# Optimization experiments

Hardware: AMD Instinct MI355X
Metric: run time of the kernel (lower is better)

## Reference

```python
import jax, jax.numpy as jnp
import numpy as np

H = 16        # num_attention_heads
KV = 4        # num_key_value_heads
HD = 128      # head_dim = hidden // H
N_REP = H // KV
ROPE_THETA = 10000.0


def _rope_cos_sin(T, dtype):
    inv_freq = 1.0 / (ROPE_THETA ** (jnp.arange(0, HD, 2, dtype=jnp.float32) / HD))
    pos = jnp.arange(T, dtype=jnp.float32)
    freqs = pos[:, None] * inv_freq[None, :]            # [T, HD/2]
    emb = jnp.concatenate([freqs, freqs], axis=-1)      # [T, HD]
    return jnp.cos(emb).astype(dtype), jnp.sin(emb).astype(dtype)


def _rotate_half(t):
    t1, t2 = jnp.split(t, 2, axis=-1)
    return jnp.concatenate([-t2, t1], axis=-1)


def setup_inputs() -> dict:
    key = jax.random.key(0)
    k1, k2, k3 = jax.random.split(key, 3)
    B, T, C = 2, 2048, 2048
    x = jax.random.normal(k1, (B, T, C), dtype=jnp.float32)
    attention_mask = jnp.ones((B, T), dtype=jnp.float32)
    w_qkv = jax.random.normal(k2, ((H + 2 * KV) * HD, C), dtype=jnp.float32) * 0.02
    w_proj = jax.random.normal(k3, (C, C), dtype=jnp.float32) * 0.02
    return {"x": x, "attention_mask": attention_mask, "w_qkv": w_qkv, "w_proj": w_proj}


def reference(x, attention_mask, w_qkv, w_proj):
    B, T, C = x.shape
    dtype = x.dtype
    neg = jnp.finfo(dtype).min

    # additive mask: causal (-big above diagonal) + padding ((1-mask)*min)
    i = jnp.arange(T)
    causal = jnp.where(i[None, :] <= i[:, None], 0.0, neg).astype(dtype)  # [T,T]
    add_mask = (1.0 - attention_mask)[:, None, None, :] * neg + causal[None, None]  # [B,1,T,T]

    # fused QKV projection
    qkv = jnp.einsum('btc,oc->bto', x, w_qkv)
    q = qkv[..., : H * HD].reshape(B, T, H, HD)
    k = qkv[..., H * HD : (H + KV) * HD].reshape(B, T, KV, HD)
    v = qkv[..., (H + KV) * HD :].reshape(B, T, KV, HD)

    # RoPE on q and k
    cos, sin = _rope_cos_sin(T, dtype)
    cos = cos[None, :, None, :]
    sin = sin[None, :, None, :]
    q = q * cos + _rotate_half(q) * sin
    k = k * cos + _rotate_half(k) * sin

    # GQA: repeat_interleave KV heads
    k = jnp.repeat(k, N_REP, axis=2)  # [B,T,H,HD]
    v = jnp.repeat(v, N_REP, axis=2)

    # [B,H,T,HD]
    q, k, v = (jnp.transpose(t, (0, 2, 1, 3)) for t in (q, k, v))

    scores = jnp.einsum('bhqd,bhkd->bhqk', q, k) * (1.0 / np.sqrt(HD))
    att = jax.nn.softmax(scores + add_mask, axis=-1)
    y = jnp.einsum('bhqk,bhkd->bhqd', att, v)
    y = jnp.transpose(y, (0, 2, 1, 3)).reshape(B, T, C)
    return jnp.einsum('btc,oc->bto', y, w_proj)
```

## Files before the change

kernel.cpp:

```cpp
#include <hip/hip_runtime.h>
#include <hip/hip_bf16.h>
#include <stdint.h>

typedef unsigned short u16;
typedef __attribute__((ext_vector_type(4))) float f32x4;
typedef __attribute__((ext_vector_type(16))) float f32x16;
typedef __attribute__((ext_vector_type(8))) __bf16 bf16x8;

#define NB 2
#define NT 2048
#define NC 2048
#define NH 16
#define NKV 4
#define HD 128
#define NQKV 3072
#define SCALE2 0.12751739f

__device__ __forceinline__ u16 f2bf(float f) {
  union { float f; uint32_t u; } c; c.f = f;
  uint32_t u = c.u + 0x7fffu + ((c.u >> 16) & 1u);
  return (u16)(u >> 16);
}
__device__ __forceinline__ float bf2f(u16 h) {
  union { uint32_t u; float f; } c; c.u = ((uint32_t)h) << 16;
  return c.f;
}
__device__ __forceinline__ uint32_t packbf2(float a, float b) {
  return (uint32_t)f2bf(a) | ((uint32_t)f2bf(b) << 16);
}

__device__ __forceinline__ void gload16(const void* g, void* lds) {
  __builtin_amdgcn_global_load_lds(
      (__attribute__((address_space(1))) void*)(uintptr_t)g,
      (__attribute__((address_space(3))) void*)(uint32_t)(uintptr_t)lds,
      16, 0, 0);
}

__global__ void cvt_bf16_kernel(const float* __restrict__ in, u16* __restrict__ out, int n4) {
  int i = blockIdx.x * blockDim.x + threadIdx.x;
  if (i >= n4) return;
  float4 v = ((const float4*)in)[i];
  uint32_t lo = (uint32_t)f2bf(v.x) | ((uint32_t)f2bf(v.y) << 16);
  uint32_t hi = (uint32_t)f2bf(v.z) | ((uint32_t)f2bf(v.w) << 16);
  ((uint2*)out)[i] = make_uint2(lo, hi);
}

__global__ void rope_tab_kernel(float* __restrict__ tab) {
  int idx = blockIdx.x * blockDim.x + threadIdx.x;
  int t = idx >> 6, i = idx & 63;
  float inv = expf(-(float)(2 * i) * (9.210340371976184f / 128.f));
  float f = (float)t * inv;
  tab[t * 128 + i] = cosf(f);
  tab[t * 128 + 64 + i] = sinf(f);
}

__global__ void rope_apply_kernel(const u16* __restrict__ qkv, const float* __restrict__ tab,
                                  u16* __restrict__ Q, u16* __restrict__ K) {
  int idx = blockIdx.x * blockDim.x + threadIdx.x;
  int i = idx & 63;
  int rest = idx >> 6;
  int hh = rest % 20;
  int bt = rest / 20;
  int t = bt & (NT - 1);
  int b = bt >> 11;
  const u16* src_row = qkv + (long)bt * NQKV;
  float c = tab[t * 128 + i], s = tab[t * 128 + 64 + i];
  if (hh < NH) {
    const u16* sp = src_row + hh * HD;
    float x0 = bf2f(sp[i]), x1 = bf2f(sp[i + 64]);
    u16* dp = Q + ((long)(b * NH + hh) * NT + t) * HD;
    dp[i] = f2bf((x0 * c - x1 * s) * SCALE2);
    dp[i + 64] = f2bf((x1 * c + x0 * s) * SCALE2);
  } else {
    int kh = hh - NH;
    const u16* sp = src_row + (NH + kh) * HD;
    float x0 = bf2f(sp[i]), x1 = bf2f(sp[i + 64]);
    u16* dp = K + ((long)(b * NKV + kh) * NT + t) * HD;
    dp[i] = f2bf(x0 * c - x1 * s);
    dp[i + 64] = f2bf(x1 * c + x0 * s);
  }
}

__global__ void vtrans_kernel(const u16* __restrict__ qkv, u16* __restrict__ Vt) {
  __shared__ u16 tile[64][72];
  const int t0 = (blockIdx.x >> 1) * 64;
  const int d0 = (blockIdx.x & 1) * 64;
  const int bkh = blockIdx.y;
  const int tid = threadIdx.x;
  const int tr = tid >> 2;
  const int tc = (tid & 3) * 16;
  const u16* src = qkv + ((long)((bkh >> 2) * NT) + t0 + tr) * NQKV +
                   (NH + NKV) * HD + (bkh & 3) * HD + d0 + tc;
  uint4 v0 = *(const uint4*)(src);
  uint4 v1 = *(const uint4*)(src + 8);
  *(uint4*)&tile[tr][tc] = v0;
  *(uint4*)&tile[tr][tc + 8] = v1;
  __syncthreads();
  const int dr = tid >> 2;
  const int tcc = (tid & 3) * 16;
  uint32_t pk[8];
#pragma unroll
  for (int e = 0; e < 8; ++e) {
    u16 a = tile[tcc + 2 * e][dr];
    u16 bq = tile[tcc + 2 * e + 1][dr];
    pk[e] = (uint32_t)a | ((uint32_t)bq << 16);
  }
  uint32_t tmp;
  tmp = pk[2]; pk[2] = pk[4]; pk[4] = tmp;
  tmp = pk[3]; pk[3] = pk[5]; pk[5] = tmp;
  const int d = d0 + dr;
  const int t = t0 + tcc;
  u16* dst = Vt + (long)bkh * HD * NT + (long)(d >> 1) * (2 * NT) +
             (t >> 6) * 128 + (d & 1) * 64 + (t & 48);
  *(uint4*)(dst) = *(uint4*)&pk[0];
  *(uint4*)(dst + 8) = *(uint4*)&pk[4];
}

template <int OUT_BF16, int NREP>
__global__ __launch_bounds__(512, 1) void gemm256_kernel(const u16* __restrict__ A,
                                                         const u16* __restrict__ Bm,
                                                         void* __restrict__ Cm,
                                                         int M, int N, int K) {
  constexpr int BN = NREP * 32;
  __shared__ __align__(16) u16 As[2][256 * 64];
  __shared__ __align__(16) u16 Bs[2][BN * 64];
  const int tid = threadIdx.x, lane = tid & 63, wid = tid >> 6;
  const int wr = wid >> 1, wc = wid & 1;
  const int g = lane >> 4, r = lane & 15;
  const long row0 = (long)blockIdx.y * 256;
  const long col0 = (long)blockIdx.x * BN;
  const int lrow = lane >> 3;
  const int lch = lane & 7;

  f32x4 acc[4][NREP] = {};

  auto stage = [&](int bufi, int kt) {
    const int k0 = kt * 64;
    u16* Ad = As[bufi];
    u16* Bd = Bs[bufi];
#pragma unroll
    for (int ii = 0; ii < 4; ++ii) {
      int rowl = wid * 32 + ii * 8 + lrow;
      const u16* src = A + (row0 + rowl) * (long)K + k0 + ((lch ^ (rowl & 7)) * 8);
      gload16(src, Ad + (wid * 32 + ii * 8) * 64);
    }
#pragma unroll
    for (int ii = 0; ii < NREP / 2; ++ii) {
      int rowl = wid * (NREP * 4) + ii * 8 + lrow;
      const u16* src = Bm + (col0 + rowl) * (long)K + k0 + ((lch ^ (rowl & 7)) * 8);
      gload16(src, Bd + (wid * (NREP * 4) + ii * 8) * 64);
    }
  };

  const int nt = K / 64;
  stage(0, 0);
  int buf = 0;
  for (int t = 0; t < nt; ++t) {
    if (t + 1 < nt) {
      stage(buf ^ 1, t + 1);
      __builtin_amdgcn_sched_barrier(0);
      if constexpr (NREP == 4) {
        asm volatile("s_waitcnt vmcnt(6)" ::: "memory");
      } else {
        asm volatile("s_waitcnt vmcnt(7)" ::: "memory");
      }
    } else {
      __builtin_amdgcn_sched_barrier(0);
      asm volatile("s_waitcnt vmcnt(0)" ::: "memory");
    }
    __builtin_amdgcn_sched_barrier(0);
    __builtin_amdgcn_s_barrier();
    __builtin_amdgcn_sched_barrier(0);

    const char* Ab = (const char*)As[buf];
    const char* Bb = (const char*)Bs[buf];
#pragma unroll
    for (int ks = 0; ks < 2; ++ks) {
      bf16x8 af[4], bfv[NREP];
#pragma unroll
      for (int mi = 0; mi < 4; ++mi) {
        int row = wr * 64 + mi * 16 + r;
        af[mi] = *(const bf16x8*)(Ab + row * 128 + (((4 * ks + g) ^ (row & 7)) * 16));
      }
#pragma unroll
      for (int ni = 0; ni < NREP; ++ni) {
        int row = wc * (NREP * 16) + ni * 16 + r;
        bfv[ni] = *(const bf16x8*)(Bb + row * 128 + (((4 * ks + g) ^ (row & 7)) * 16));
      }
      __builtin_amdgcn_s_setprio(1);
#pragma unroll
      for (int mi = 0; mi < 4; ++mi)
#pragma unroll
        for (int ni = 0; ni < NREP; ++ni)
          acc[mi][ni] = __builtin_amdgcn_mfma_f32_16x16x32_bf16(af[mi], bfv[ni], acc[mi][ni], 0, 0, 0);
      __builtin_amdgcn_s_setprio(0);
    }
    __builtin_amdgcn_sched_barrier(0);
    __builtin_amdgcn_s_barrier();
    __builtin_amdgcn_sched_barrier(0);
    buf ^= 1;
  }

#pragma unroll
  for (int mi = 0; mi < 4; ++mi)
#pragma unroll
    for (int ni = 0; ni < NREP; ++ni)
#pragma unroll
      for (int j = 0; j < 4; ++j) {
        long rr = row0 + wr * 64 + mi * 16 + g * 4 + j;
        long cc = col0 + wc * (NREP * 16) + ni * 16 + r;
        float v = acc[mi][ni][j];
        if (OUT_BF16) ((u16*)Cm)[rr * N + cc] = f2bf(v);
        else          ((float*)Cm)[rr * N + cc] = v;
      }
}

__global__ __launch_bounds__(256, 2) void attn_kernel(const u16* __restrict__ Qg,
                                                      const u16* __restrict__ Kg,
                                                      const u16* __restrict__ Vtg,
                                                      const float* __restrict__ amask,
                                                      u16* __restrict__ Y) {
  __shared__ __align__(16) u16 Ks[2][64 * 128];
  __shared__ __align__(16) u16 Vs[2][64 * 128];
  const int tid = threadIdx.x, lane = tid & 63, wid = tid >> 6;
  const int ql = lane & 31, hi = lane >> 5;
  const int id = blockIdx.x;
  const int h = id & 15;
  const int xp = (id >> 4) & 7;
  const int b = (id >> 7) & 1;
  const int half = id >> 8;
  const int qt = half ? 15 - xp : xp;
  const int q0 = qt * 128;
  const int kh = h >> 2;

  const u16* Kbh = Kg + (long)(b * NKV + kh) * NT * HD;
  const u16* Vtbh = Vtg + (long)(b * NKV + kh) * HD * NT;
  const u16* Qbh = Qg + (long)(b * NH + h) * NT * HD;
  const float* am_b = amask + b * NT;

  const int total = 2 * qt + 2;

  const int srow = lane >> 4;
  const int schunk = lane & 15;
  auto stageK = [&](u16* dst, int kv0) {
#pragma unroll
    for (int ii = 0; ii < 4; ++ii) {
      int kvl = wid * 16 + ii * 4 + srow;
      const u16* src = Kbh + (long)(kv0 + kvl) * HD + ((schunk ^ (kvl & 15)) * 8);
      gload16(src, dst + (wid * 16 + ii * 4) * 128);
    }
  };
  auto stageV = [&](u16* dst, int kv0) {
    const u16* vb = Vtbh + (kv0 >> 6) * 128;
#pragma unroll
    for (int ii = 0; ii < 4; ++ii) {
      int R = wid * 16 + ii * 4 + srow;
      const u16* src = vb + (long)R * (2 * NT) + ((schunk ^ (R & 15)) * 8);
      gload16(src, dst + (wid * 16 + ii * 4) * 128);
    }
  };

  bf16x8 qf[8];
  {
    const u16* Qrow = Qbh + (long)(q0 + wid * 32 + ql) * HD;
#pragma unroll
    for (int ks = 0; ks < 8; ++ks)
      qf[ks] = *(const bf16x8*)(Qrow + ks * 16 + 8 * hi);
  }

  stageK(Ks[0], 0);
  stageV(Vs[0], 0);
  __syncthreads();

  float m = -INFINITY;
  f32x4 lacc = {};
  f32x16 o[4] = {};
  int buf = 0;
  const int qi = q0 + wid * 32 + ql;

  for (int i = 0; i < total; ++i) {
    const int kv0 = i * 64;

    if (i + 1 < total) {
      stageK(Ks[buf ^ 1], (i + 1) * 64);
      stageV(Vs[buf ^ 1], (i + 1) * 64);
    }

    const char* Ksb = (const char*)Ks[buf];
    const char* Vsb = (const char*)Vs[buf];

    f32x16 s0a = {}, s0b = {}, s1a = {}, s1b = {};
    __builtin_amdgcn_s_setprio(1);
#pragma unroll
    for (int ks = 0; ks < 4; ++ks) {
      bf16x8 kf0 = *(const bf16x8*)(Ksb + ql * 256 + (((2 * ks + hi) ^ (ql & 15)) * 16));
      bf16x8 kf1 = *(const bf16x8*)(Ksb + (32 + ql) * 256 + (((2 * ks + hi) ^ (ql & 15)) * 16));
      s0a = __builtin_amdgcn_mfma_f32_32x32x16_bf16(kf0, qf[ks], s0a, 0, 0, 0);
      s1a = __builtin_amdgcn_mfma_f32_32x32x16_bf16(kf1, qf[ks], s1a, 0, 0, 0);
    }
#pragma unroll
    for (int ks = 4; ks < 8; ++ks) {
      bf16x8 kf0 = *(const bf16x8*)(Ksb + ql * 256 + (((2 * ks + hi) ^ (ql & 15)) * 16));
      bf16x8 kf1 = *(const bf16x8*)(Ksb + (32 + ql) * 256 + (((2 * ks + hi) ^ (ql & 15)) * 16));
      s0b = __builtin_amdgcn_mfma_f32_32x32x16_bf16(kf0, qf[ks], s0b, 0, 0, 0);
      s1b = __builtin_amdgcn_mfma_f32_32x32x16_bf16(kf1, qf[ks], s1b, 0, 0, 0);
    }
    __builtin_amdgcn_s_setprio(0);
    f32x16 s0 = s0a + s0b;
    f32x16 s1 = s1a + s1b;

    if (i >= 2 * qt) {
#pragma unroll
      for (int reg = 0; reg < 16; ++reg) {
        int kvl = (reg & 3) + 8 * (reg >> 2) + 4 * hi;
        if (kv0 + kvl > qi) s0[reg] = -INFINITY;
        if (kv0 + 32 + kvl > qi) s1[reg] = -INFINITY;
      }
    }

    float t16[16];
#pragma unroll
    for (int reg = 0; reg < 16; ++reg) t16[reg] = fmaxf(s0[reg], s1[reg]);
    float t8[8];
#pragma unroll
    for (int reg = 0; reg < 8; ++reg) t8[reg] = fmaxf(t16[reg], t16[reg + 8]);
    float t4[4];
#pragma unroll
    for (int reg = 0; reg < 4; ++reg) t4[reg] = fmaxf(t8[reg], t8[reg + 4]);
    float mxl = fmaxf(fmaxf(t4[0], t4[1]), fmaxf(t4[2], t4[3]));
    if (!__all(mxl <= m + 8.f)) {
      float mx = fmaxf(mxl, __shfl_xor(mxl, 32));
      float mnew = fmaxf(m, mx);
      float alpha = exp2f(m - mnew);
      m = mnew;
      lacc *= alpha;
#pragma unroll
      for (int dblk = 0; dblk < 4; ++dblk) o[dblk] *= alpha;
    }

    float4 am0[4], am1[4];
#pragma unroll
    for (int uu = 0; uu < 4; ++uu) {
      am0[uu] = *(const float4*)(am_b + kv0 + 8 * uu + 4 * hi);
      am1[uu] = *(const float4*)(am_b + kv0 + 32 + 8 * uu + 4 * hi);
    }
#pragma unroll
    for (int reg = 0; reg < 16; ++reg) {
      float p0 = exp2f(s0[reg] - m) * (&am0[reg >> 2].x)[reg & 3];
      float p1 = exp2f(s1[reg] - m) * (&am1[reg >> 2].x)[reg & 3];
      s0[reg] = p0; s1[reg] = p1;
      lacc[reg & 3] += p0 + p1;
    }

    bf16x8 pb[4];
#pragma unroll
    for (int ks = 0; ks < 4; ++ks) {
      union { __bf16 hh[8]; bf16x8 v; } pk;
      const int base = 8 * (ks & 1);
#pragma unroll
      for (int j = 0; j < 8; ++j)
        pk.hh[j] = (__bf16)((ks >= 2) ? s1[base + j] : s0[base + j]);
      pb[ks] = pk.v;
    }

    __builtin_amdgcn_s_setprio(1);
#pragma unroll
    for (int ks = 0; ks < 4; ++ks) {
#pragma unroll
      for (int dblk = 0; dblk < 4; ++dblk) {
        int drow = dblk * 16 + (ql >> 1);
        int gr = ((ql & 1) * 8 + 2 * ks + hi) ^ (drow & 15);
        bf16x8 va = *(const bf16x8*)(Vsb + drow * 256 + gr * 16);
        o[dblk] = __builtin_amdgcn_mfma_f32_32x32x16_bf16(va, pb[ks], o[dblk], 0, 0, 0);
      }
    }
    __builtin_amdgcn_s_setprio(0);

    __syncthreads();
    buf ^= 1;
  }

  {
    float l = (lacc[0] + lacc[1]) + (lacc[2] + lacc[3]);
    l += __shfl_xor(l, 32);
    float invl = 1.f / l;
    u16* Yrow = Y + ((long)b * NT + qi) * NC + h * HD;
#pragma unroll
    for (int dblk = 0; dblk < 4; ++dblk)
#pragma unroll
      for (int uu = 0; uu < 4; ++uu) {
        int d = dblk * 32 + 8 * uu + 4 * hi;
        int r0 = 4 * uu;
        *(uint2*)(Yrow + d) = make_uint2(
            packbf2(o[dblk][r0] * invl, o[dblk][r0 + 1] * invl),
            packbf2(o[dblk][r0 + 2] * invl, o[dblk][r0 + 3] * invl));
      }
  }
}

extern "C" void kernel_launch(void* const* d_in, const int* in_sizes, int n_in,
                              void* d_out, int out_size, void* d_ws, size_t ws_size,
                              hipStream_t stream) {
  const float* x = (const float*)d_in[0];
  const float* amask = (const float*)d_in[1];
  const float* w_qkv = (const float*)d_in[2];
  const float* w_proj = (const float*)d_in[3];

  const long MT = (long)NB * NT;
  char* ws = (char*)d_ws;
  size_t off = 0;
  auto carve = [&](size_t bytes) -> char* {
    char* p = ws + off;
    off += (bytes + 255) & ~(size_t)255;
    return p;
  };
  u16* xb   = (u16*)carve((size_t)MT * NC * 2);
  u16* wqb  = (u16*)carve((size_t)NQKV * NC * 2);
  u16* wpb  = (u16*)carve((size_t)NC * NC * 2);
  u16* qkvb = (u16*)carve((size_t)MT * NQKV * 2);
  float* tab = (float*)carve((size_t)NT * 128 * 4);

  u16* Qb = xb;
  u16* Kb = wqb;
  u16* Vtb = wqb + (size_t)NB * NKV * NT * HD;
  u16* Yb = qkvb;

  {
    int n4 = (int)(MT * NC / 4);
    cvt_bf16_kernel<<<dim3((n4 + 255) / 256), dim3(256), 0, stream>>>(x, xb, n4);
    n4 = (int)((long)NQKV * NC / 4);
    cvt_bf16_kernel<<<dim3((n4 + 255) / 256), dim3(256), 0, stream>>>(w_qkv, wqb, n4);
    n4 = (int)((long)NC * NC / 4);
    cvt_bf16_kernel<<<dim3((n4 + 255) / 256), dim3(256), 0, stream>>>(w_proj, wpb, n4);
  }
  rope_tab_kernel<<<dim3(NT * 64 / 256), dim3(256), 0, stream>>>(tab);
  gemm256_kernel<1, 6><<<dim3(NQKV / 192, MT / 256), dim3(512), 0, stream>>>(xb, wqb, qkvb, (int)MT, NQKV, NC);
  rope_apply_kernel<<<dim3(NB * NT * 20 * 64 / 256), dim3(256), 0, stream>>>(qkvb, tab, Qb, Kb);
  vtrans_kernel<<<dim3(NT / 64 * 2, NB * NKV), dim3(256), 0, stream>>>(qkvb, Vtb);
  attn_kernel<<<dim3(512), dim3(256), 0, stream>>>(Qb, Kb, Vtb, amask, Yb);
  gemm256_kernel<0, 4><<<dim3(NC / 128, MT / 256), dim3(512), 0, stream>>>(Yb, wpb, d_out, (int)MT, NC, NC);
}
```

Before: 200.4 us.

## Split long causal attention tiles across two KV partitions with combine pass

For the query tiles in the upper half (qt 8-15), the KV loop is split into two blocks that each process half the KV range. They write unnormalised bf16 partial outputs plus the running max and sum, and a new combine kernel merges them with log-sum-exp rescaling. This aims to balance causal work across more workgroups (768 instead of 512) so the long-tail tiles no longer set the critical path. It costs extra global traffic for the partials, an additional kernel launch, and some precision loss from storing partials in bf16. The split path only runs if the workspace is large enough to hold the partial buffers.

```diff
diff --git a/kernel.cpp b/kernel.cpp
--- a/kernel.cpp
+++ b/kernel.cpp
@@ -219,17 +219,34 @@
                                                       const u16* __restrict__ Kg,
                                                       const u16* __restrict__ Vtg,
                                                       const float* __restrict__ amask,
-                                                      u16* __restrict__ Y) {
+                                                      u16* __restrict__ Y,
+                                                      u16* __restrict__ Op,
+                                                      float* __restrict__ Lm,
+                                                      int split_en) {
   __shared__ __align__(16) u16 Ks[2][64 * 128];
   __shared__ __align__(16) u16 Vs[2][64 * 128];
   const int tid = threadIdx.x, lane = tid & 63, wid = tid >> 6;
   const int ql = lane & 31, hi = lane >> 5;
   const int id = blockIdx.x;
-  const int h = id & 15;
-  const int xp = (id >> 4) & 7;
-  const int b = (id >> 7) & 1;
-  const int half = id >> 8;
-  const int qt = half ? 15 - xp : xp;
+  int h, qt, b, kvlo, kvhi, part;
+  if (!split_en) {
+    h = id & 15;
+    int xp = (id >> 4) & 7;
+    b = (id >> 7) & 1;
+    qt = (id >> 8) ? 15 - xp : xp;
+    kvlo = 0; kvhi = 2 * qt + 2; part = -1;
+  } else if (id < 256) {
+    h = id & 15; qt = (id >> 4) & 7; b = id >> 7;
+    kvlo = 0; kvhi = 2 * qt + 2; part = -1;
+  } else {
+    int j = id - 256;
+    part = j >> 8;
+    int k = j & 255;
+    h = k & 15; qt = 8 + ((k >> 4) & 7); b = k >> 7;
+    int n = 2 * qt + 2, n0 = qt + 1;
+    kvlo = part ? n0 : 0;
+    kvhi = part ? n : n0;
+  }
   const int q0 = qt * 128;
   const int kh = h >> 2;
 
@@ -238,8 +255,6 @@
   const u16* Qbh = Qg + (long)(b * NH + h) * NT * HD;
   const float* am_b = amask + b * NT;
 
-  const int total = 2 * qt + 2;
-
   const int srow = lane >> 4;
   const int schunk = lane & 15;
   auto stageK = [&](u16* dst, int kv0) {
@@ -268,8 +283,8 @@
       qf[ks] = *(const bf16x8*)(Qrow + ks * 16 + 8 * hi);
   }
 
-  stageK(Ks[0], 0);
-  stageV(Vs[0], 0);
+  stageK(Ks[0], kvlo * 64);
+  stageV(Vs[0], kvlo * 64);
   __syncthreads();
 
   float m = -INFINITY;
@@ -278,10 +293,10 @@
   int buf = 0;
   const int qi = q0 + wid * 32 + ql;
 
-  for (int i = 0; i < total; ++i) {
+  for (int i = kvlo; i < kvhi; ++i) {
     const int kv0 = i * 64;
 
-    if (i + 1 < total) {
+    if (i + 1 < kvhi) {
       stageK(Ks[buf ^ 1], (i + 1) * 64);
       stageV(Vs[buf ^ 1], (i + 1) * 64);
     }
@@ -383,18 +398,64 @@
   {
     float l = (lacc[0] + lacc[1]) + (lacc[2] + lacc[3]);
     l += __shfl_xor(l, 32);
-    float invl = 1.f / l;
-    u16* Yrow = Y + ((long)b * NT + qi) * NC + h * HD;
-#pragma unroll
-    for (int dblk = 0; dblk < 4; ++dblk)
-#pragma unroll
-      for (int uu = 0; uu < 4; ++uu) {
-        int d = dblk * 32 + 8 * uu + 4 * hi;
-        int r0 = 4 * uu;
-        *(uint2*)(Yrow + d) = make_uint2(
-            packbf2(o[dblk][r0] * invl, o[dblk][r0 + 1] * invl),
-            packbf2(o[dblk][r0 + 2] * invl, o[dblk][r0 + 3] * invl));
-      }
+    if (part < 0) {
+      float invl = 1.f / l;
+      u16* Yrow = Y + ((long)b * NT + qi) * NC + h * HD;
+#pragma unroll
+      for (int dblk = 0; dblk < 4; ++dblk)
+#pragma unroll
+        for (int uu = 0; uu < 4; ++uu) {
+          int d = dblk * 32 + 8 * uu + 4 * hi;
+          int r0 = 4 * uu;
+          *(uint2*)(Yrow + d) = make_uint2(
+              packbf2(o[dblk][r0] * invl, o[dblk][r0 + 1] * invl),
+              packbf2(o[dblk][r0 + 2] * invl, o[dblk][r0 + 3] * invl));
+        }
+    } else {
+      const int inst = ((b * 16 + h) << 3) + (qt - 8);
+      const long rbase = (long)(part * 256 + inst) * 128 + wid * 32 + ql;
+      u16* Orow = Op + rbase * 128;
+#pragma unroll
+      for (int dblk = 0; dblk < 4; ++dblk)
+#pragma unroll
+        for (int uu = 0; uu < 4; ++uu) {
+          int d = dblk * 32 + 8 * uu + 4 * hi;
+          int r0 = 4 * uu;
+          *(uint2*)(Orow + d) = make_uint2(
+              packbf2(o[dblk][r0], o[dblk][r0 + 1]),
+              packbf2(o[dblk][r0 + 2], o[dblk][r0 + 3]));
+        }
+      if (hi == 0) *(float2*)(Lm + rbase * 2) = make_float2(m, l);
+    }
+  }
+}
+
+__global__ __launch_bounds__(256) void attn_combine_kernel(const u16* __restrict__ Op,
+                                                           const float* __restrict__ Lm,
+                                                           u16* __restrict__ Y) {
+  const int k = blockIdx.x, tid = threadIdx.x;
+  const int b = k >> 7, h = (k >> 3) & 15, qtm8 = k & 7;
+  const int row = tid >> 1, dbase = (tid & 1) * 64;
+  const long r0 = (long)k * 128 + row;
+  const long r1 = (long)(256 + k) * 128 + row;
+  float2 ml0 = *(const float2*)(Lm + r0 * 2);
+  float2 ml1 = *(const float2*)(Lm + r1 * 2);
+  float M = fmaxf(ml0.x, ml1.x);
+  float a0 = exp2f(ml0.x - M), a1 = exp2f(ml1.x - M);
+  float invl = 1.f / (a0 * ml0.y + a1 * ml1.y);
+  a0 *= invl; a1 *= invl;
+  const u16* p0 = Op + r0 * 128 + dbase;
+  const u16* p1 = Op + r1 * 128 + dbase;
+  u16* Yrow = Y + ((long)b * NT + (qtm8 + 8) * 128 + row) * NC + h * HD + dbase;
+#pragma unroll
+  for (int e = 0; e < 8; ++e) {
+    union { uint4 u; u16 hh[8]; } A, B2, O2;
+    A.u = *(const uint4*)(p0 + e * 8);
+    B2.u = *(const uint4*)(p1 + e * 8);
+#pragma unroll
+    for (int j = 0; j < 8; ++j)
+      O2.hh[j] = f2bf(a0 * bf2f(A.hh[j]) + a1 * bf2f(B2.hh[j]));
+    *(uint4*)(Yrow + e * 8) = O2.u;
   }
 }
 
@@ -419,6 +480,9 @@
   u16* wpb  = (u16*)carve((size_t)NC * NC * 2);
   u16* qkvb = (u16*)carve((size_t)MT * NQKV * 2);
   float* tab = (float*)carve((size_t)NT * 128 * 4);
+  u16* Op   = (u16*)carve((size_t)2 * 256 * 128 * 128 * 2);
+  float* Lm = (float*)carve((size_t)2 * 256 * 128 * 2 * 4);
+  const bool use_split = (off <= ws_size);
 
   u16* Qb = xb;
   u16* Kb = wqb;
@@ -437,6 +501,11 @@
   gemm256_kernel<1, 6><<<dim3(NQKV / 192, MT / 256), dim3(512), 0, stream>>>(xb, wqb, qkvb, (int)MT, NQKV, NC);
   rope_apply_kernel<<<dim3(NB * NT * 20 * 64 / 256), dim3(256), 0, stream>>>(qkvb, tab, Qb, Kb);
   vtrans_kernel<<<dim3(NT / 64 * 2, NB * NKV), dim3(256), 0, stream>>>(qkvb, Vtb);
-  attn_kernel<<<dim3(512), dim3(256), 0, stream>>>(Qb, Kb, Vtb, amask, Yb);
+  if (use_split) {
+    attn_kernel<<<dim3(768), dim3(256), 0, stream>>>(Qb, Kb, Vtb, amask, Yb, Op, Lm, 1);
+    attn_combine_kernel<<<dim3(256), dim3(256), 0, stream>>>(Op, Lm, Yb);
+  } else {
+    attn_kernel<<<dim3(512), dim3(256), 0, stream>>>(Qb, Kb, Vtb, amask, Yb, Op, Lm, 0);
+  }
   gemm256_kernel<0, 4><<<dim3(NC / 128, MT / 256), dim3(512), 0, stream>>>(Yb, wpb, d_out, (int)MT, NC, NC);
 }
```

Result: slower. 216.6 us (+8.1%).
